# Kernel optimization log

Hardware: AMD Instinct MI355X
Metric: run time of the kernel (lower is better)

The kernel has to match this reference:

```python
import jax, jax.numpy as jnp
import numpy as np

N_NODES = 1024  # cities (fully connected graph)
N_HID = 128     # config.N: edge-MLP hidden dim (W2: N_HID x 3)
M = 128         # config.M: embedding dim
T = 4           # config.T: message-passing iterations
TAU = 10.0      # config.tau: softmax temperature


def setup_inputs() -> dict:
    key = jax.random.key(0)
    ks = jax.random.split(key, 18)
    u = lambda k, s: jax.random.uniform(k, s, dtype=jnp.float32)
    return dict(
        D=u(ks[0], (N_NODES, N_NODES)),       # pairwise distances graph[v][u]
        dd=u(ks[1], (N_NODES,)),              # graph[depot][v]
        dr=u(ks[2], (N_NODES,)),              # distance_from_robot()
        ddep=u(ks[3], (N_NODES,)),            # distance_from_depot()
        mu0_A1=u(ks[4], (N_NODES, M)),
        mu0_A2=u(ks[5], (N_NODES, M)),
        mu0_B=u(ks[6], (N_NODES, M)),
        W1=u(ks[7], (1, N_HID)),
        W2=u(ks[8], (N_HID, 3)),
        W3_A1=u(ks[9], (M, M + 1)),
        W3_A2=u(ks[10], (M, M + 1)),
        W4_A1=u(ks[11], (M, 1)),
        W4_A2=u(ks[12], (M, 1)),
        W3_B=u(ks[13], (M, M)),
        W4_B=u(ks[14], (M, 2 * M)),
        W5=u(ks[15], (1, M)),
        W6=u(ks[16], (1, M)),
        W7=u(ks[17], (1, M)),
    )


def _edge_scores(D, dd, W1, W2):
    # G[v,u] = W1 @ relu(W2 @ [D[v,u], dd[v], dd[u]])  -> scalar per pair
    h = (D[:, :, None] * W2[:, 0]
         + dd[:, None, None] * W2[:, 1]
         + dd[None, :, None] * W2[:, 2])            # (n, n, N_HID)
    return jnp.maximum(h, 0.0) @ W1[0]              # (n, n)


def _attn(G):
    # p[u,v] = softmax over sources u != v of G[u,v]/tau
    n = G.shape[0]
    Gm = jnp.where(jnp.eye(n, dtype=bool), -jnp.inf, G / TAU)
    return jax.nn.softmax(Gm, axis=0)


def _layer_A(P, wd, mu, Wg, W3, W4, dist):
    # l_v = [ sum_u p_uv * D[u,v] * relu(Wg @ mu_v) ; sum_u p_uv * mu_u ]
    # mu_v <- relu(W3 @ l_v + W4 * dist_v)
    for _ in range(T):
        s = jnp.maximum(mu @ Wg[0], 0.0)                        # (n,)
        l = jnp.concatenate([(wd * s)[:, None], P.T @ mu], 1)   # (n, M+1)
        mu = jnp.maximum(l @ W3.T + dist[:, None] * W4[:, 0][None, :], 0.0)
    return mu


def reference(D, dd, dr, ddep, mu0_A1, mu0_A2, mu0_B,
              W1, W2, W3_A1, W3_A2, W4_A1, W4_A2, W3_B, W4_B, W5, W6, W7):
    # A1 and B use distances / 1000 for edge scores; A2 uses raw distances.
    G_scaled = _edge_scores(D / 1000.0, dd / 1000.0, W1, W2)
    G_raw = _edge_scores(D, dd, W1, W2)
    P1 = _attn(G_scaled)
    P2 = _attn(G_raw)
    wd1 = jnp.sum(P1 * D, axis=0)   # attention-weighted raw edge distance, per v
    wd2 = jnp.sum(P2 * D, axis=0)

    A1 = _layer_A(P1, wd1, mu0_A1, W5, W3_A1, W4_A1, dr)
    A2 = _layer_A(P2, wd2, mu0_A2, W6, W3_A2, W4_A2, ddep)

    bias = jnp.concatenate([A1, A2], axis=1) @ W4_B.T  # (n, M), constant over t
    mu = mu0_B
    for _ in range(T):
        mu = jnp.maximum((P1.T @ mu) @ W3_B.T + bias, 0.0)

    return jnp.maximum(W7 @ jnp.sum(mu, axis=0)[:, None], 0.0)  # (1, 1)
```

## Files before the change

kernel.cpp:

```cpp
#include <hip/hip_runtime.h>
#include <math.h>

#define N 1024
#define M 128

typedef unsigned short us16;

__device__ __forceinline__ us16 f2bf(float f) {
  unsigned int u = __float_as_uint(f);
  unsigned int r = u + 0x7FFFu + ((u >> 16) & 1u);
  return (us16)(r >> 16);
}
__device__ __forceinline__ float bf2f(us16 u) {
  return __uint_as_float(((unsigned int)u) << 16);
}

__global__ __launch_bounds__(256) void k_prep(
    const float* __restrict__ D, float* __restrict__ DT,
    const float* __restrict__ W3A1, const float* __restrict__ W3A2,
    const float* __restrict__ W3B, const float* __restrict__ W4B,
    float* __restrict__ W3A1T, float* __restrict__ W3A2T,
    float* __restrict__ W3BT, float* __restrict__ W4BT,
    const float* __restrict__ mu0A1, const float* __restrict__ mu0A2,
    const float* __restrict__ mu0B,
    const float* __restrict__ W5, const float* __restrict__ W6,
    float* __restrict__ s1, float* __restrict__ s2,
    us16* __restrict__ muA1_0, us16* __restrict__ muA2_0, us16* __restrict__ muB_0,
    float* __restrict__ gsum, unsigned int* __restrict__ gcnt) {
  int bx = blockIdx.x, t = threadIdx.x;
  if (bx < 1024) {
    __shared__ float tile[32 * 33];
    int tx = t & 31, ty = t >> 5;
    int bxx = (bx & 31) * 32, by = (bx >> 5) * 32;
#pragma unroll
    for (int i = 0; i < 4; i++)
      tile[(ty + i * 8) * 33 + tx] = D[(size_t)(by + ty + i * 8) * N + bxx + tx];
    __syncthreads();
#pragma unroll
    for (int i = 0; i < 4; i++)
      DT[(size_t)(bxx + ty + i * 8) * N + by + tx] = tile[tx * 33 + ty + i * 8];
  } else if (bx < 1345) {
    int idx = (bx - 1024) * 256 + t;
    const float* in = nullptr; float* op = nullptr; int cols = 0, o = 0;
    if (idx < 16512)      { in = W3A1; op = W3A1T; cols = 129; o = idx; }
    else if (idx < 33024) { in = W3A2; op = W3A2T; cols = 129; o = idx - 16512; }
    else if (idx < 49408) { in = W3B;  op = W3BT;  cols = 128; o = idx - 33024; }
    else if (idx < 82176) { in = W4B;  op = W4BT;  cols = 256; o = idx - 49408; }
    if (in) { int r = o & 127, c = o >> 7; op[o] = in[r * cols + c]; }
  } else if (bx < 1473) {
    int idx = (bx - 1345) * 256 + t;
    int row = idx >> 4, l16 = idx & 15;
    int chain = row >> 10, r = row & 1023;
    const float* mu0 = chain ? mu0A2 : mu0A1;
    const float* Wg = chain ? W6 : W5;
    float* sb = chain ? s2 : s1;
    const float* mp = mu0 + (size_t)r * M + l16 * 8;
    float4 a0 = *(const float4*)mp, a1 = *(const float4*)(mp + 4);
    float4 g0 = *(const float4*)(Wg + l16 * 8), g1 = *(const float4*)(Wg + l16 * 8 + 4);
    float sp = a0.x * g0.x + a0.y * g0.y + a0.z * g0.z + a0.w * g0.w
             + a1.x * g1.x + a1.y * g1.y + a1.z * g1.z + a1.w * g1.w;
#pragma unroll
    for (int o = 8; o; o >>= 1) sp += __shfl_xor(sp, o);
    if (l16 == 0) sb[r] = sp;
  } else if (bx < 1857) {
    int idx = (bx - 1473) * 256 + t;
    int mat = idx >> 15, o4 = idx & 32767;
    const float* src = mat == 0 ? mu0A1 : (mat == 1 ? mu0A2 : mu0B);
    us16* dst = mat == 0 ? muA1_0 : (mat == 1 ? muA2_0 : muB_0);
    float4 v = *(const float4*)(src + (size_t)o4 * 4);
    ushort4 p;
    p.x = f2bf(v.x); p.y = f2bf(v.y); p.z = f2bf(v.z); p.w = f2bf(v.w);
    *(ushort4*)(dst + (size_t)o4 * 4) = p;
  } else {
    if (t == 0) { *gsum = 0.f; *gcnt = 0u; }
  }
}

__device__ __forceinline__ float blk_max(float v, float* red, int t) {
#pragma unroll
  for (int o = 32; o; o >>= 1) v = fmaxf(v, __shfl_xor(v, o));
  __syncthreads();
  if ((t & 63) == 0) red[t >> 6] = v;
  __syncthreads();
  return fmaxf(fmaxf(red[0], red[1]), fmaxf(red[2], red[3]));
}
__device__ __forceinline__ float blk_sum(float v, float* red, int t) {
#pragma unroll
  for (int o = 32; o; o >>= 1) v += __shfl_xor(v, o);
  __syncthreads();
  if ((t & 63) == 0) red[t >> 6] = v;
  __syncthreads();
  return red[0] + red[1] + red[2] + red[3];
}

__global__ __launch_bounds__(256) void k_edge(const float* __restrict__ DT,
                                              const float* __restrict__ dd,
                                              const float* __restrict__ W1,
                                              const float* __restrict__ W2,
                                              us16* __restrict__ PT1bf, us16* __restrict__ PT2bf,
                                              float* __restrict__ wd1, float* __restrict__ wd2) {
  __shared__ float4 wp[128];
  __shared__ float red[4];
  int t = threadIdx.x, v = blockIdx.x;
  if (t < 128) {
    float4 p;
    p.x = W2[t * 3 + 0]; p.y = W2[t * 3 + 1]; p.z = W2[t * 3 + 2]; p.w = W1[t];
    wp[t] = p;
  }
  __syncthreads();
  float yv = dd[v];
  float4 xv = *(const float4*)&DT[(size_t)v * N + t * 4];
  float4 zv = *(const float4*)&dd[t * 4];
  float x[4] = {xv.x, xv.y, xv.z, xv.w};
  float z[4] = {zv.x, zv.y, zv.z, zv.w};
  float g[4] = {0.f, 0.f, 0.f, 0.f};
#pragma unroll 2
  for (int k = 0; k < 128; k++) {
    float4 wk = wp[k];
    float cv = yv * wk.z;
#pragma unroll
    for (int i = 0; i < 4; i++) {
      float h = fmaf(x[i], wk.x, fmaf(z[i], wk.y, cv));
      g[i] = fmaf(fmaxf(h, 0.f), wk.w, g[i]);
    }
  }
#pragma unroll
  for (int i = 0; i < 4; i++)
    if (t * 4 + i == v) g[i] = -INFINITY;
  float m = fmaxf(fmaxf(g[0], g[1]), fmaxf(g[2], g[3]));
  m = blk_max(m, red, t);
  float er[4], es[4], sr = 0.f, ss = 0.f;
#pragma unroll
  for (int i = 0; i < 4; i++) {
    er[i] = expf((g[i] - m) * 0.1f);
    es[i] = expf((g[i] - m) * 1e-4f);
    sr += er[i]; ss += es[i];
  }
  sr = blk_sum(sr, red, t);
  ss = blk_sum(ss, red, t);
  float ir = 1.f / sr, is = 1.f / ss;
  float ps0 = es[0] * is, ps1 = es[1] * is, ps2 = es[2] * is, ps3 = es[3] * is;
  float pr0 = er[0] * ir, pr1 = er[1] * ir, pr2 = er[2] * ir, pr3 = er[3] * ir;
  ushort4 p1, p2;
  p1.x = f2bf(ps0); p1.y = f2bf(ps1); p1.z = f2bf(ps2); p1.w = f2bf(ps3);
  p2.x = f2bf(pr0); p2.y = f2bf(pr1); p2.z = f2bf(pr2); p2.w = f2bf(pr3);
  *(ushort4*)(PT1bf + (size_t)v * N + t * 4) = p1;
  *(ushort4*)(PT2bf + (size_t)v * N + t * 4) = p2;
  float a1 = ps0 * x[0] + ps1 * x[1] + ps2 * x[2] + ps3 * x[3];
  float a2 = pr0 * x[0] + pr1 * x[1] + pr2 * x[2] + pr3 * x[3];
  a1 = blk_sum(a1, red, t);
  a2 = blk_sum(a2, red, t);
  if (t == 0) { wd1[v] = a1; wd2[v] = a2; }
}

__device__ __forceinline__ void gemm4_bf(const us16* __restrict__ PTbf,
                                         const us16* __restrict__ curbf,
                                         float* __restrict__ As, float* __restrict__ CsP,
                                         int r0, int t) {
#pragma unroll
  for (int i = 0; i < 4; i++) {
    int idx = t + i * 256;
    int row = idx >> 8, c4 = idx & 255;
    ushort4 a = *(const ushort4*)(PTbf + (size_t)(r0 + row) * N + c4 * 4);
    float4 f;
    f.x = bf2f(a.x); f.y = bf2f(a.y); f.z = bf2f(a.z); f.w = bf2f(a.w);
    *(float4*)&As[row * 1024 + c4 * 4] = f;
  }
  __syncthreads();
  const int kc = t >> 5;
  const int cg = t & 31;
  const int u0 = kc * 128;
  float4 acc0 = {0,0,0,0}, acc1 = {0,0,0,0}, acc2 = {0,0,0,0}, acc3 = {0,0,0,0};
  const us16* mub = curbf + (size_t)u0 * M + cg * 4;
  const float* a0p = As + u0;
  const float* a1p = As + 1024 + u0;
  const float* a2p = As + 2048 + u0;
  const float* a3p = As + 3072 + u0;
#pragma unroll 2
  for (int uu = 0; uu < 128; uu += 4) {
    float4 a0 = *(const float4*)&a0p[uu];
    float4 a1 = *(const float4*)&a1p[uu];
    float4 a2 = *(const float4*)&a2p[uu];
    float4 a3 = *(const float4*)&a3p[uu];
    ushort4 v0 = *(const ushort4*)&mub[(size_t)(uu + 0) * M];
    ushort4 v1 = *(const ushort4*)&mub[(size_t)(uu + 1) * M];
    ushort4 v2 = *(const ushort4*)&mub[(size_t)(uu + 2) * M];
    ushort4 v3 = *(const ushort4*)&mub[(size_t)(uu + 3) * M];
    float4 b0 = {bf2f(v0.x), bf2f(v0.y), bf2f(v0.z), bf2f(v0.w)};
    float4 b1 = {bf2f(v1.x), bf2f(v1.y), bf2f(v1.z), bf2f(v1.w)};
    float4 b2 = {bf2f(v2.x), bf2f(v2.y), bf2f(v2.z), bf2f(v2.w)};
    float4 b3 = {bf2f(v3.x), bf2f(v3.y), bf2f(v3.z), bf2f(v3.w)};
#define FMA4(ACC, AV) \
    ACC.x = fmaf(AV.x, b0.x, ACC.x); ACC.y = fmaf(AV.x, b0.y, ACC.y); \
    ACC.z = fmaf(AV.x, b0.z, ACC.z); ACC.w = fmaf(AV.x, b0.w, ACC.w); \
    ACC.x = fmaf(AV.y, b1.x, ACC.x); ACC.y = fmaf(AV.y, b1.y, ACC.y); \
    ACC.z = fmaf(AV.y, b1.z, ACC.z); ACC.w = fmaf(AV.y, b1.w, ACC.w); \
    ACC.x = fmaf(AV.z, b2.x, ACC.x); ACC.y = fmaf(AV.z, b2.y, ACC.y); \
    ACC.z = fmaf(AV.z, b2.z, ACC.z); ACC.w = fmaf(AV.z, b2.w, ACC.w); \
    ACC.x = fmaf(AV.w, b3.x, ACC.x); ACC.y = fmaf(AV.w, b3.y, ACC.y); \
    ACC.z = fmaf(AV.w, b3.z, ACC.z); ACC.w = fmaf(AV.w, b3.w, ACC.w);
    FMA4(acc0, a0) FMA4(acc1, a1) FMA4(acc2, a2) FMA4(acc3, a3)
#undef FMA4
  }
  float* cp = CsP + kc * 512 + cg * 4;
  *(float4*)&cp[0]   = acc0;
  *(float4*)&cp[128] = acc1;
  *(float4*)&cp[256] = acc2;
  *(float4*)&cp[384] = acc3;
  __syncthreads();
#pragma unroll
  for (int i = 0; i < 2; i++) {
    int j = t + i * 256;
    float s = 0.f;
#pragma unroll
    for (int s8 = 0; s8 < 8; s8++) s += CsP[s8 * 512 + j];
    As[j] = s;
  }
  __syncthreads();
}

__global__ __launch_bounds__(256) void k_iterA(
    const us16* __restrict__ PT1bf, const us16* __restrict__ PT2bf,
    const us16* __restrict__ cur1, const us16* __restrict__ cur2,
    const us16* __restrict__ curB0,
    us16* __restrict__ nxt1, us16* __restrict__ nxt2, float* __restrict__ CB0f,
    float* __restrict__ s1buf, float* __restrict__ s2buf,
    const float* __restrict__ wd1, const float* __restrict__ wd2,
    const float* __restrict__ dr, const float* __restrict__ ddep,
    const float* __restrict__ W3A1T, const float* __restrict__ W3A2T,
    const float* __restrict__ W3BT,
    const float* __restrict__ W4A1, const float* __restrict__ W4A2,
    const float* __restrict__ W5, const float* __restrict__ W6) {
  __shared__ float smem[8192];
  float* As = smem;
  float* CsP = smem + 4096;
  const int z = blockIdx.z;
  const int t = threadIdx.x, r0 = blockIdx.x * 4;
  const us16* PT = (z == 1) ? PT2bf : PT1bf;
  const us16* cur = (z == 0) ? cur1 : (z == 1) ? cur2 : curB0;

  gemm4_bf(PT, cur, As, CsP, r0, t);

  const float* W3T = (z == 0) ? W3A1T : (z == 1) ? W3A2T : W3BT;
  int col = t & 127, ra = t >> 7;
  float accA = 0.f, accB = 0.f;
  const float* wcol = W3T + (z < 2 ? 128 : 0) + col;
#pragma unroll 4
  for (int m = 0; m < 128; m += 4) {
    float4 c0 = *(const float4*)&As[ra * 128 + m];
    float4 c1 = *(const float4*)&As[(ra + 2) * 128 + m];
    float w0 = wcol[(m + 0) * 128], w1 = wcol[(m + 1) * 128];
    float w2 = wcol[(m + 2) * 128], w3 = wcol[(m + 3) * 128];
    accA = fmaf(c0.x, w0, fmaf(c0.y, w1, fmaf(c0.z, w2, fmaf(c0.w, w3, accA))));
    accB = fmaf(c1.x, w0, fmaf(c1.y, w1, fmaf(c1.z, w2, fmaf(c1.w, w3, accB))));
  }
  int rA = r0 + ra, rB = r0 + ra + 2;
  if (z == 2) {
    CB0f[(size_t)rA * M + col] = accA;
    CB0f[(size_t)rB * M + col] = accB;
    return;
  }
  float* sbuf = z ? s2buf : s1buf;
  const float* wdv = z ? wd2 : wd1;
  const float* dist = z ? ddep : dr;
  const float* W4c = z ? W4A2 : W4A1;
  const float* Wg = z ? W6 : W5;
  us16* nxt = z ? nxt2 : nxt1;
  float w30 = W3T[col], w4 = W4c[col];
  float svA = wdv[rA] * fmaxf(sbuf[rA], 0.f);
  float svB = wdv[rB] * fmaxf(sbuf[rB], 0.f);
  float o0 = fmaxf(fmaf(svA, w30, fmaf(dist[rA], w4, accA)), 0.f);
  float o1 = fmaxf(fmaf(svB, w30, fmaf(dist[rB], w4, accB)), 0.f);
  nxt[(size_t)rA * M + col] = f2bf(o0);
  nxt[(size_t)rB * M + col] = f2bf(o1);
  __syncthreads();
  CsP[ra * 128 + col] = o0;
  CsP[(ra + 2) * 128 + col] = o1;
  __syncthreads();
  if (t < 64) {
    int row = t >> 4, l16 = t & 15;
    const float* cr = &CsP[row * 128 + l16 * 8];
    float4 x0 = *(const float4*)cr, x1 = *(const float4*)(cr + 4);
    float4 g0 = *(const float4*)(Wg + l16 * 8), g1 = *(const float4*)(Wg + l16 * 8 + 4);
    float sp = x0.x * g0.x + x0.y * g0.y + x0.z * g0.z + x0.w * g0.w
             + x1.x * g1.x + x1.y * g1.y + x1.z * g1.z + x1.w * g1.w;
#pragma unroll
    for (int o = 8; o; o >>= 1) sp += __shfl_xor(sp, o);
    if (l16 == 0) sbuf[r0 + row] = sp;
  }
}

__global__ __launch_bounds__(256) void k_bmerge(
    const us16* __restrict__ A1bf, const us16* __restrict__ A2bf,
    const float* __restrict__ W4BT, const float* __restrict__ CB0f,
    float* __restrict__ biasb, us16* __restrict__ muB1) {
  int t = threadIdx.x, r0 = blockIdx.x * 4;
  int col = t & 127, ra = t >> 7;
  int rA = r0 + ra, rB = r0 + ra + 2;
  float b0 = 0.f, b1 = 0.f;
  const us16* a1a = A1bf + (size_t)rA * M;
  const us16* a1b = A1bf + (size_t)rB * M;
  const us16* a2a = A2bf + (size_t)rA * M;
  const us16* a2b = A2bf + (size_t)rB * M;
#pragma unroll 4
  for (int c = 0; c < 128; c++) {
    float wv = W4BT[c * 128 + col];
    b0 = fmaf(bf2f(a1a[c]), wv, b0);
    b1 = fmaf(bf2f(a1b[c]), wv, b1);
  }
#pragma unroll 4
  for (int c = 0; c < 128; c++) {
    float wv = W4BT[(c + 128) * 128 + col];
    b0 = fmaf(bf2f(a2a[c]), wv, b0);
    b1 = fmaf(bf2f(a2b[c]), wv, b1);
  }
  biasb[(size_t)rA * M + col] = b0;
  biasb[(size_t)rB * M + col] = b1;
  muB1[(size_t)rA * M + col] = f2bf(fmaxf(CB0f[(size_t)rA * M + col] + b0, 0.f));
  muB1[(size_t)rB * M + col] = f2bf(fmaxf(CB0f[(size_t)rB * M + col] + b1, 0.f));
}

__global__ __launch_bounds__(256) void k_iterB(
    const us16* __restrict__ PT1bf, const us16* __restrict__ curbf,
    us16* __restrict__ nxtbf,
    const float* __restrict__ W3BT, const float* __restrict__ biasb,
    const float* __restrict__ W7, float* __restrict__ gsum,
    unsigned int* __restrict__ gcnt, float* __restrict__ out, int last) {
  __shared__ float smem[8192];
  __shared__ float redf[4];
  float* As = smem;
  float* CsP = smem + 4096;
  int t = threadIdx.x, r0 = blockIdx.x * 4;
  gemm4_bf(PT1bf, curbf, As, CsP, r0, t);
  int col = t & 127, ra = t >> 7;
  float accA = 0.f, accB = 0.f;
  const float* wcol = W3BT + col;
#pragma unroll 4
  for (int m = 0; m < 128; m += 4) {
    float4 c0 = *(const float4*)&As[ra * 128 + m];
    float4 c1 = *(const float4*)&As[(ra + 2) * 128 + m];
    float w0 = wcol[(m + 0) * 128], w1 = wcol[(m + 1) * 128];
    float w2 = wcol[(m + 2) * 128], w3 = wcol[(m + 3) * 128];
    accA = fmaf(c0.x, w0, fmaf(c0.y, w1, fmaf(c0.z, w2, fmaf(c0.w, w3, accA))));
    accB = fmaf(c1.x, w0, fmaf(c1.y, w1, fmaf(c1.z, w2, fmaf(c1.w, w3, accB))));
  }
  int rA = r0 + ra, rB = r0 + ra + 2;
  float o0 = fmaxf(accA + biasb[(size_t)rA * M + col], 0.f);
  float o1 = fmaxf(accB + biasb[(size_t)rB * M + col], 0.f);
  if (!last) {
    nxtbf[(size_t)rA * M + col] = f2bf(o0);
    nxtbf[(size_t)rB * M + col] = f2bf(o1);
  } else {
    float s = (o0 + o1) * W7[col];
#pragma unroll
    for (int off = 32; off; off >>= 1) s += __shfl_xor(s, off);
    if ((t & 63) == 0) redf[t >> 6] = s;
    __syncthreads();
    if (t == 0) {
      float bs = redf[0] + redf[1] + redf[2] + redf[3];
      atomicAdd(gsum, bs);
      __threadfence();
      unsigned int old = atomicAdd(gcnt, 1u);
      if (old == 255u) {
        float tot = atomicAdd(gsum, 0.f);
        out[0] = fmaxf(tot, 0.f);
      }
    }
  }
}

extern "C" void kernel_launch(void* const* d_in, const int* in_sizes, int n_in,
                              void* d_out, int out_size, void* d_ws, size_t ws_size,
                              hipStream_t stream) {
  (void)in_sizes; (void)n_in; (void)out_size; (void)ws_size;
  const float* D     = (const float*)d_in[0];
  const float* dd    = (const float*)d_in[1];
  const float* dr    = (const float*)d_in[2];
  const float* ddep  = (const float*)d_in[3];
  const float* mu0A1 = (const float*)d_in[4];
  const float* mu0A2 = (const float*)d_in[5];
  const float* mu0B  = (const float*)d_in[6];
  const float* W1    = (const float*)d_in[7];
  const float* W2    = (const float*)d_in[8];
  const float* W3A1  = (const float*)d_in[9];
  const float* W3A2  = (const float*)d_in[10];
  const float* W4A1  = (const float*)d_in[11];
  const float* W4A2  = (const float*)d_in[12];
  const float* W3B   = (const float*)d_in[13];
  const float* W4B   = (const float*)d_in[14];
  const float* W5    = (const float*)d_in[15];
  const float* W6    = (const float*)d_in[16];
  const float* W7    = (const float*)d_in[17];

  float* wsf = (float*)d_ws;
  size_t o = 0;
  auto alloc = [&](size_t n) { float* p = wsf + o; o += n; return p; };
  float* DT     = alloc((size_t)N * N);
  us16* PT1bf   = (us16*)alloc((size_t)N * N / 2);
  us16* PT2bf   = (us16*)alloc((size_t)N * N / 2);
  float* W3A1T  = alloc(129 * 128);
  float* W3A2T  = alloc(129 * 128);
  float* W3BT   = alloc(128 * 128);
  float* W4BT   = alloc(256 * 128);
  float* s1     = alloc(N);
  float* s2     = alloc(N);
  float* wd1    = alloc(N);
  float* wd2    = alloc(N);
  us16* muA1_0  = (us16*)alloc((size_t)N * M / 2);
  us16* muA1_a  = (us16*)alloc((size_t)N * M / 2);
  us16* muA1_b  = (us16*)alloc((size_t)N * M / 2);
  us16* muA2_0  = (us16*)alloc((size_t)N * M / 2);
  us16* muA2_a  = (us16*)alloc((size_t)N * M / 2);
  us16* muA2_b  = (us16*)alloc((size_t)N * M / 2);
  us16* muB_0   = (us16*)alloc((size_t)N * M / 2);
  us16* muB_a   = (us16*)alloc((size_t)N * M / 2);
  us16* muB_b   = (us16*)alloc((size_t)N * M / 2);
  float* CB0f   = alloc((size_t)N * M);
  float* biasb  = alloc((size_t)N * M);
  float* gsum   = alloc(1);
  unsigned int* gcnt = (unsigned int*)alloc(1);

  k_prep<<<1858, 256, 0, stream>>>(D, DT, W3A1, W3A2, W3B, W4B,
                                   W3A1T, W3A2T, W3BT, W4BT,
                                   mu0A1, mu0A2, mu0B, W5, W6, s1, s2,
                                   muA1_0, muA2_0, muB_0, gsum, gcnt);
  k_edge<<<N, 256, 0, stream>>>(DT, dd, W1, W2, PT1bf, PT2bf, wd1, wd2);

  const us16* c1 = muA1_0;
  const us16* c2 = muA2_0;
  us16* b1[2] = {muA1_a, muA1_b};
  us16* b2[2] = {muA2_a, muA2_b};
  for (int it = 0; it < 4; it++) {
    dim3 grid(256, 1, it == 0 ? 3 : 2);
    k_iterA<<<grid, 256, 0, stream>>>(PT1bf, PT2bf, c1, c2, muB_0,
        b1[it & 1], b2[it & 1], CB0f, s1, s2, wd1, wd2, dr, ddep,
        W3A1T, W3A2T, W3BT, W4A1, W4A2, W5, W6);
    c1 = b1[it & 1];
    c2 = b2[it & 1];
  }

  k_bmerge<<<256, 256, 0, stream>>>(muA1_b, muA2_b, W4BT, CB0f, biasb, muB_a);

  const us16* cB = muB_a;
  us16* bB[2] = {muB_b, muB_a};
  for (int i = 0; i < 3; i++) {
    k_iterB<<<256, 256, 0, stream>>>(PT1bf, cB, bB[i & 1],
        W3BT, biasb, W7, gsum, gcnt, (float*)d_out, i == 2 ? 1 : 0);
    cB = bB[i & 1];
  }
}
```

Measured before the change: 152.3 us.

## Fuse edge-score kernel into prep and merge last A-iteration with bias merge

```diff
diff --git a/kernel.cpp b/kernel.cpp
--- a/kernel.cpp
+++ b/kernel.cpp
@@ -15,8 +15,28 @@
   return __uint_as_float(((unsigned int)u) << 16);
 }
 
-__global__ __launch_bounds__(256) void k_prep(
-    const float* __restrict__ D, float* __restrict__ DT,
+__device__ __forceinline__ float blk_max(float v, float* red, int t) {
+#pragma unroll
+  for (int o = 32; o; o >>= 1) v = fmaxf(v, __shfl_xor(v, o));
+  __syncthreads();
+  if ((t & 63) == 0) red[t >> 6] = v;
+  __syncthreads();
+  return fmaxf(fmaxf(red[0], red[1]), fmaxf(red[2], red[3]));
+}
+__device__ __forceinline__ float blk_sum(float v, float* red, int t) {
+#pragma unroll
+  for (int o = 32; o; o >>= 1) v += __shfl_xor(v, o);
+  __syncthreads();
+  if ((t & 63) == 0) red[t >> 6] = v;
+  __syncthreads();
+  return red[0] + red[1] + red[2] + red[3];
+}
+
+__global__ __launch_bounds__(256) void k_edge_prep(
+    const float* __restrict__ D, const float* __restrict__ dd,
+    const float* __restrict__ W1, const float* __restrict__ W2,
+    us16* __restrict__ PT1bf, us16* __restrict__ PT2bf,
+    float* __restrict__ wd1, float* __restrict__ wd2,
     const float* __restrict__ W3A1, const float* __restrict__ W3A2,
     const float* __restrict__ W3B, const float* __restrict__ W4B,
     float* __restrict__ W3A1T, float* __restrict__ W3A2T,
@@ -27,18 +47,61 @@
     float* __restrict__ s1, float* __restrict__ s2,
     us16* __restrict__ muA1_0, us16* __restrict__ muA2_0, us16* __restrict__ muB_0,
     float* __restrict__ gsum, unsigned int* __restrict__ gcnt) {
+  __shared__ float4 wp[128];
+  __shared__ float red[4];
   int bx = blockIdx.x, t = threadIdx.x;
   if (bx < 1024) {
-    __shared__ float tile[32 * 33];
-    int tx = t & 31, ty = t >> 5;
-    int bxx = (bx & 31) * 32, by = (bx >> 5) * 32;
+    int v = bx;
+    if (t < 128) {
+      float4 p;
+      p.x = W2[t * 3 + 0]; p.y = W2[t * 3 + 1]; p.z = W2[t * 3 + 2]; p.w = W1[t];
+      wp[t] = p;
+    }
+    __syncthreads();
+    float yv = dd[v];
+    float x[4], z[4], g[4] = {0.f, 0.f, 0.f, 0.f};
 #pragma unroll
     for (int i = 0; i < 4; i++)
-      tile[(ty + i * 8) * 33 + tx] = D[(size_t)(by + ty + i * 8) * N + bxx + tx];
-    __syncthreads();
+      x[i] = D[(size_t)(t * 4 + i) * N + v];
+    float4 zv = *(const float4*)&dd[t * 4];
+    z[0] = zv.x; z[1] = zv.y; z[2] = zv.z; z[3] = zv.w;
+#pragma unroll 2
+    for (int k = 0; k < 128; k++) {
+      float4 wk = wp[k];
+      float cv = yv * wk.z;
+#pragma unroll
+      for (int i = 0; i < 4; i++) {
+        float h = fmaf(x[i], wk.x, fmaf(z[i], wk.y, cv));
+        g[i] = fmaf(fmaxf(h, 0.f), wk.w, g[i]);
+      }
+    }
 #pragma unroll
     for (int i = 0; i < 4; i++)
-      DT[(size_t)(bxx + ty + i * 8) * N + by + tx] = tile[tx * 33 + ty + i * 8];
+      if (t * 4 + i == v) g[i] = -INFINITY;
+    float m = fmaxf(fmaxf(g[0], g[1]), fmaxf(g[2], g[3]));
+    m = blk_max(m, red, t);
+    float er[4], es[4], sr = 0.f, ss = 0.f;
+#pragma unroll
+    for (int i = 0; i < 4; i++) {
+      er[i] = expf((g[i] - m) * 0.1f);
+      es[i] = expf((g[i] - m) * 1e-4f);
+      sr += er[i]; ss += es[i];
+    }
+    sr = blk_sum(sr, red, t);
+    ss = blk_sum(ss, red, t);
+    float ir = 1.f / sr, is = 1.f / ss;
+    float ps0 = es[0] * is, ps1 = es[1] * is, ps2 = es[2] * is, ps3 = es[3] * is;
+    float pr0 = er[0] * ir, pr1 = er[1] * ir, pr2 = er[2] * ir, pr3 = er[3] * ir;
+    ushort4 p1, p2;
+    p1.x = f2bf(ps0); p1.y = f2bf(ps1); p1.z = f2bf(ps2); p1.w = f2bf(ps3);
+    p2.x = f2bf(pr0); p2.y = f2bf(pr1); p2.z = f2bf(pr2); p2.w = f2bf(pr3);
+    *(ushort4*)(PT1bf + (size_t)v * N + t * 4) = p1;
+    *(ushort4*)(PT2bf + (size_t)v * N + t * 4) = p2;
+    float a1 = ps0 * x[0] + ps1 * x[1] + ps2 * x[2] + ps3 * x[3];
+    float a2 = pr0 * x[0] + pr1 * x[1] + pr2 * x[2] + pr3 * x[3];
+    a1 = blk_sum(a1, red, t);
+    a2 = blk_sum(a2, red, t);
+    if (t == 0) { wd1[v] = a1; wd2[v] = a2; }
   } else if (bx < 1345) {
     int idx = (bx - 1024) * 256 + t;
     const float* in = nullptr; float* op = nullptr; int cols = 0, o = 0;
@@ -74,83 +137,6 @@
   } else {
     if (t == 0) { *gsum = 0.f; *gcnt = 0u; }
   }
-}
-
-__device__ __forceinline__ float blk_max(float v, float* red, int t) {
-#pragma unroll
-  for (int o = 32; o; o >>= 1) v = fmaxf(v, __shfl_xor(v, o));
-  __syncthreads();
-  if ((t & 63) == 0) red[t >> 6] = v;
-  __syncthreads();
-  return fmaxf(fmaxf(red[0], red[1]), fmaxf(red[2], red[3]));
-}
-__device__ __forceinline__ float blk_sum(float v, float* red, int t) {
-#pragma unroll
-  for (int o = 32; o; o >>= 1) v += __shfl_xor(v, o);
-  __syncthreads();
-  if ((t & 63) == 0) red[t >> 6] = v;
-  __syncthreads();
-  return red[0] + red[1] + red[2] + red[3];
-}
-
-__global__ __launch_bounds__(256) void k_edge(const float* __restrict__ DT,
-                                              const float* __restrict__ dd,
-                                              const float* __restrict__ W1,
-                                              const float* __restrict__ W2,
-                                              us16* __restrict__ PT1bf, us16* __restrict__ PT2bf,
-                                              float* __restrict__ wd1, float* __restrict__ wd2) {
-  __shared__ float4 wp[128];
-  __shared__ float red[4];
-  int t = threadIdx.x, v = blockIdx.x;
-  if (t < 128) {
-    float4 p;
-    p.x = W2[t * 3 + 0]; p.y = W2[t * 3 + 1]; p.z = W2[t * 3 + 2]; p.w = W1[t];
-    wp[t] = p;
-  }
-  __syncthreads();
-  float yv = dd[v];
-  float4 xv = *(const float4*)&DT[(size_t)v * N + t * 4];
-  float4 zv = *(const float4*)&dd[t * 4];
-  float x[4] = {xv.x, xv.y, xv.z, xv.w};
-  float z[4] = {zv.x, zv.y, zv.z, zv.w};
-  float g[4] = {0.f, 0.f, 0.f, 0.f};
-#pragma unroll 2
-  for (int k = 0; k < 128; k++) {
-    float4 wk = wp[k];
-    float cv = yv * wk.z;
-#pragma unroll
-    for (int i = 0; i < 4; i++) {
-      float h = fmaf(x[i], wk.x, fmaf(z[i], wk.y, cv));
-      g[i] = fmaf(fmaxf(h, 0.f), wk.w, g[i]);
-    }
-  }
-#pragma unroll
-  for (int i = 0; i < 4; i++)
-    if (t * 4 + i == v) g[i] = -INFINITY;
-  float m = fmaxf(fmaxf(g[0], g[1]), fmaxf(g[2], g[3]));
-  m = blk_max(m, red, t);
-  float er[4], es[4], sr = 0.f, ss = 0.f;
-#pragma unroll
-  for (int i = 0; i < 4; i++) {
-    er[i] = expf((g[i] - m) * 0.1f);
-    es[i] = expf((g[i] - m) * 1e-4f);
-    sr += er[i]; ss += es[i];
-  }
-  sr = blk_sum(sr, red, t);
-  ss = blk_sum(ss, red, t);
-  float ir = 1.f / sr, is = 1.f / ss;
-  float ps0 = es[0] * is, ps1 = es[1] * is, ps2 = es[2] * is, ps3 = es[3] * is;
-  float pr0 = er[0] * ir, pr1 = er[1] * ir, pr2 = er[2] * ir, pr3 = er[3] * ir;
-  ushort4 p1, p2;
-  p1.x = f2bf(ps0); p1.y = f2bf(ps1); p1.z = f2bf(ps2); p1.w = f2bf(ps3);
-  p2.x = f2bf(pr0); p2.y = f2bf(pr1); p2.z = f2bf(pr2); p2.w = f2bf(pr3);
-  *(ushort4*)(PT1bf + (size_t)v * N + t * 4) = p1;
-  *(ushort4*)(PT2bf + (size_t)v * N + t * 4) = p2;
-  float a1 = ps0 * x[0] + ps1 * x[1] + ps2 * x[2] + ps3 * x[3];
-  float a2 = pr0 * x[0] + pr1 * x[1] + pr2 * x[2] + pr3 * x[3];
-  a1 = blk_sum(a1, red, t);
-  a2 = blk_sum(a2, red, t);
-  if (t == 0) { wd1[v] = a1; wd2[v] = a2; }
 }
 
 __device__ __forceinline__ void gemm4_bf(const us16* __restrict__ PTbf,
@@ -219,6 +205,21 @@
   __syncthreads();
 }
 
+__device__ __forceinline__ void epi_mm(const float* __restrict__ Cred,
+                                       const float* __restrict__ wcol,
+                                       int ra, float& accA, float& accB) {
+  accA = 0.f; accB = 0.f;
+#pragma unroll 4
+  for (int m = 0; m < 128; m += 4) {
+    float4 c0 = *(const float4*)&Cred[ra * 128 + m];
+    float4 c1 = *(const float4*)&Cred[(ra + 2) * 128 + m];
+    float w0 = wcol[(m + 0) * 128], w1 = wcol[(m + 1) * 128];
+    float w2 = wcol[(m + 2) * 128], w3 = wcol[(m + 3) * 128];
+    accA = fmaf(c0.x, w0, fmaf(c0.y, w1, fmaf(c0.z, w2, fmaf(c0.w, w3, accA))));
+    accB = fmaf(c1.x, w0, fmaf(c1.y, w1, fmaf(c1.z, w2, fmaf(c1.w, w3, accB))));
+  }
+}
+
 __global__ __launch_bounds__(256) void k_iterA(
     const us16* __restrict__ PT1bf, const us16* __restrict__ PT2bf,
     const us16* __restrict__ cur1, const us16* __restrict__ cur2,
@@ -243,17 +244,8 @@
 
   const float* W3T = (z == 0) ? W3A1T : (z == 1) ? W3A2T : W3BT;
   int col = t & 127, ra = t >> 7;
-  float accA = 0.f, accB = 0.f;
-  const float* wcol = W3T + (z < 2 ? 128 : 0) + col;
-#pragma unroll 4
-  for (int m = 0; m < 128; m += 4) {
-    float4 c0 = *(const float4*)&As[ra * 128 + m];
-    float4 c1 = *(const float4*)&As[(ra + 2) * 128 + m];
-    float w0 = wcol[(m + 0) * 128], w1 = wcol[(m + 1) * 128];
-    float w2 = wcol[(m + 2) * 128], w3 = wcol[(m + 3) * 128];
-    accA = fmaf(c0.x, w0, fmaf(c0.y, w1, fmaf(c0.z, w2, fmaf(c0.w, w3, accA))));
-    accB = fmaf(c1.x, w0, fmaf(c1.y, w1, fmaf(c1.z, w2, fmaf(c1.w, w3, accB))));
-  }
+  float accA, accB;
+  epi_mm(As, W3T + (z < 2 ? 128 : 0) + col, ra, accA, accB);
   int rA = r0 + ra, rB = r0 + ra + 2;
   if (z == 2) {
     CB0f[(size_t)rA * M + col] = accA;
@@ -290,29 +282,75 @@
   }
 }
 
-__global__ __launch_bounds__(256) void k_bmerge(
-    const us16* __restrict__ A1bf, const us16* __restrict__ A2bf,
+__global__ __launch_bounds__(256) void k_iterA3(
+    const us16* __restrict__ PT1bf, const us16* __restrict__ PT2bf,
+    const us16* __restrict__ curA1, const us16* __restrict__ curA2,
+    us16* __restrict__ nxtA1, us16* __restrict__ nxtA2,
+    const float* __restrict__ s1buf, const float* __restrict__ s2buf,
+    const float* __restrict__ wd1, const float* __restrict__ wd2,
+    const float* __restrict__ dr, const float* __restrict__ ddep,
+    const float* __restrict__ W3A1T, const float* __restrict__ W3A2T,
+    const float* __restrict__ W4A1, const float* __restrict__ W4A2,
     const float* __restrict__ W4BT, const float* __restrict__ CB0f,
     float* __restrict__ biasb, us16* __restrict__ muB1) {
-  int t = threadIdx.x, r0 = blockIdx.x * 4;
+  __shared__ float smem[8192 + 512];
+  float* As = smem;
+  float* CsP = smem + 4096;
+  float* st1 = smem + 8192;
+  const int t = threadIdx.x, r0 = blockIdx.x * 4;
   int col = t & 127, ra = t >> 7;
   int rA = r0 + ra, rB = r0 + ra + 2;
+
+  gemm4_bf(PT1bf, curA1, As, CsP, r0, t);
+  {
+    float accA, accB;
+    epi_mm(As, W3A1T + 128 + col, ra, accA, accB);
+    float w30 = W3A1T[col], w4 = W4A1[col];
+    float svA = wd1[rA] * fmaxf(s1buf[rA], 0.f);
+    float svB = wd1[rB] * fmaxf(s1buf[rB], 0.f);
+    float o0 = fmaxf(fmaf(svA, w30, fmaf(dr[rA], w4, accA)), 0.f);
+    float o1 = fmaxf(fmaf(svB, w30, fmaf(dr[rB], w4, accB)), 0.f);
+    nxtA1[(size_t)rA * M + col] = f2bf(o0);
+    nxtA1[(size_t)rB * M + col] = f2bf(o1);
+    st1[ra * 128 + col] = o0;
+    st1[(ra + 2) * 128 + col] = o1;
+  }
+  __syncthreads();
+
+  gemm4_bf(PT2bf, curA2, As, CsP, r0, t);
+  {
+    float accA, accB;
+    epi_mm(As, W3A2T + 128 + col, ra, accA, accB);
+    float w30 = W3A2T[col], w4 = W4A2[col];
+    float svA = wd2[rA] * fmaxf(s2buf[rA], 0.f);
+    float svB = wd2[rB] * fmaxf(s2buf[rB], 0.f);
+    float o0 = fmaxf(fmaf(svA, w30, fmaf(ddep[rA], w4, accA)), 0.f);
+    float o1 = fmaxf(fmaf(svB, w30, fmaf(ddep[rB], w4, accB)), 0.f);
+    nxtA2[(size_t)rA * M + col] = f2bf(o0);
+    nxtA2[(size_t)rB * M + col] = f2bf(o1);
+    CsP[ra * 128 + col] = o0;
+    CsP[(ra + 2) * 128 + col] = o1;
+  }
+  __syncthreads();
+
   float b0 = 0.f, b1 = 0.f;
-  const us16* a1a = A1bf + (size_t)rA * M;
-  const us16* a1b = A1bf + (size_t)rB * M;
-  const us16* a2a = A2bf + (size_t)rA * M;
-  const us16* a2b = A2bf + (size_t)rB * M;
 #pragma unroll 4
-  for (int c = 0; c < 128; c++) {
-    float wv = W4BT[c * 128 + col];
-    b0 = fmaf(bf2f(a1a[c]), wv, b0);
-    b1 = fmaf(bf2f(a1b[c]), wv, b1);
+  for (int c = 0; c < 128; c += 4) {
+    float4 s0 = *(const float4*)&st1[ra * 128 + c];
+    float4 s1v = *(const float4*)&st1[(ra + 2) * 128 + c];
+    float w0 = W4BT[(c + 0) * 128 + col], w1 = W4BT[(c + 1) * 128 + col];
+    float w2 = W4BT[(c + 2) * 128 + col], w3 = W4BT[(c + 3) * 128 + col];
+    b0 = fmaf(s0.x, w0, fmaf(s0.y, w1, fmaf(s0.z, w2, fmaf(s0.w, w3, b0))));
+    b1 = fmaf(s1v.x, w0, fmaf(s1v.y, w1, fmaf(s1v.z, w2, fmaf(s1v.w, w3, b1))));
   }
 #pragma unroll 4
-  for (int c = 0; c < 128; c++) {
-    float wv = W4BT[(c + 128) * 128 + col];
-    b0 = fmaf(bf2f(a2a[c]), wv, b0);
-    b1 = fmaf(bf2f(a2b[c]), wv, b1);
+  for (int c = 0; c < 128; c += 4) {
+    float4 s0 = *(const float4*)&CsP[ra * 128 + c];
+    float4 s1v = *(const float4*)&CsP[(ra + 2) * 128 + c];
+    float w0 = W4BT[(c + 128) * 128 + col], w1 = W4BT[(c + 129) * 128 + col];
+    float w2 = W4BT[(c + 130) * 128 + col], w3 = W4BT[(c + 131) * 128 + col];
+    b0 = fmaf(s0.x, w0, fmaf(s0.y, w1, fmaf(s0.z, w2, fmaf(s0.w, w3, b0))));
+    b1 = fmaf(s1v.x, w0, fmaf(s1v.y, w1, fmaf(s1v.z, w2, fmaf(s1v.w, w3, b1))));
   }
   biasb[(size_t)rA * M + col] = b0;
   biasb[(size_t)rB * M + col] = b1;
@@ -333,17 +371,8 @@
   int t = threadIdx.x, r0 = blockIdx.x * 4;
   gemm4_bf(PT1bf, curbf, As, CsP, r0, t);
   int col = t & 127, ra = t >> 7;
-  float accA = 0.f, accB = 0.f;
-  const float* wcol = W3BT + col;
-#pragma unroll 4
-  for (int m = 0; m < 128; m += 4) {
-    float4 c0 = *(const float4*)&As[ra * 128 + m];
-    float4 c1 = *(const float4*)&As[(ra + 2) * 128 + m];
-    float w0 = wcol[(m + 0) * 128], w1 = wcol[(m + 1) * 128];
-    float w2 = wcol[(m + 2) * 128], w3 = wcol[(m + 3) * 128];
-    accA = fmaf(c0.x, w0, fmaf(c0.y, w1, fmaf(c0.z, w2, fmaf(c0.w, w3, accA))));
-    accB = fmaf(c1.x, w0, fmaf(c1.y, w1, fmaf(c1.z, w2, fmaf(c1.w, w3, accB))));
-  }
+  float accA, accB;
+  epi_mm(As, W3BT + col, ra, accA, accB);
   int rA = r0 + ra, rB = r0 + ra + 2;
   float o0 = fmaxf(accA + biasb[(size_t)rA * M + col], 0.f);
   float o1 = fmaxf(accB + biasb[(size_t)rB * M + col], 0.f);
@@ -395,7 +424,6 @@
   float* wsf = (float*)d_ws;
   size_t o = 0;
   auto alloc = [&](size_t n) { float* p = wsf + o; o += n; return p; };
-  float* DT     = alloc((size_t)N * N);
   us16* PT1bf   = (us16*)alloc((size_t)N * N / 2);
   us16* PT2bf   = (us16*)alloc((size_t)N * N / 2);
   float* W3A1T  = alloc(129 * 128);
@@ -420,17 +448,17 @@
   float* gsum   = alloc(1);
   unsigned int* gcnt = (unsigned int*)alloc(1);
 
-  k_prep<<<1858, 256, 0, stream>>>(D, DT, W3A1, W3A2, W3B, W4B,
-                                   W3A1T, W3A2T, W3BT, W4BT,
-                                   mu0A1, mu0A2, mu0B, W5, W6, s1, s2,
-                                   muA1_0, muA2_0, muB_0, gsum, gcnt);
-  k_edge<<<N, 256, 0, stream>>>(DT, dd, W1, W2, PT1bf, PT2bf, wd1, wd2);
+  k_edge_prep<<<1858, 256, 0, stream>>>(D, dd, W1, W2, PT1bf, PT2bf, wd1, wd2,
+                                        W3A1, W3A2, W3B, W4B,
+                                        W3A1T, W3A2T, W3BT, W4BT,
+                                        mu0A1, mu0A2, mu0B, W5, W6, s1, s2,
+                                        muA1_0, muA2_0, muB_0, gsum, gcnt);
 
   const us16* c1 = muA1_0;
   const us16* c2 = muA2_0;
   us16* b1[2] = {muA1_a, muA1_b};
   us16* b2[2] = {muA2_a, muA2_b};
-  for (int it = 0; it < 4; it++) {
+  for (int it = 0; it < 3; it++) {
     dim3 grid(256, 1, it == 0 ? 3 : 2);
     k_iterA<<<grid, 256, 0, stream>>>(PT1bf, PT2bf, c1, c2, muB_0,
         b1[it & 1], b2[it & 1], CB0f, s1, s2, wd1, wd2, dr, ddep,
@@ -439,7 +467,9 @@
     c2 = b2[it & 1];
   }
 
-  k_bmerge<<<256, 256, 0, stream>>>(muA1_b, muA2_b, W4BT, CB0f, biasb, muB_a);
+  k_iterA3<<<256, 256, 0, stream>>>(PT1bf, PT2bf, c1, c2,
+      muA1_b, muA2_b, s1, s2, wd1, wd2, dr, ddep,
+      W3A1T, W3A2T, W4A1, W4A2, W4BT, CB0f, biasb, muB_a);
 
   const us16* cB = muB_a;
   us16* bB[2] = {muB_b, muB_a};
```

Measured after the change: 143.3 us. 1.06x faster.
